# Kernel optimization log

Hardware: AMD Instinct MI355X
Metric: run time of the kernel (lower is better)

Reference implementation:

```python
import jax, jax.numpy as jnp
import numpy as np

N_SAMPLES, N_CHANNELS, LOOKBACK, N_ASSETS = 256, 32, 64, 512
HIDDEN = 32  # hidden_size == n_channels per docstring output shape


def setup_inputs() -> dict:
    key = jax.random.key(0)
    k1, k2, k3, k4, k5 = jax.random.split(key, 5)
    bound = 1.0 / np.sqrt(HIDDEN)  # torch RNNCell init: U(-1/sqrt(H), 1/sqrt(H))
    x = jax.random.normal(k1, (N_SAMPLES, N_CHANNELS, LOOKBACK, N_ASSETS), dtype=jnp.float32)
    W_ih = jax.random.uniform(k2, (HIDDEN, N_CHANNELS), jnp.float32, -bound, bound)
    W_hh = jax.random.uniform(k3, (HIDDEN, HIDDEN), jnp.float32, -bound, bound)
    b_ih = jax.random.uniform(k4, (HIDDEN,), jnp.float32, -bound, bound)
    b_hh = jax.random.uniform(k5, (HIDDEN,), jnp.float32, -bound, bound)
    return {"x": x, "W_ih": W_ih, "W_hh": W_hh, "b_ih": b_ih, "b_hh": b_hh}


def reference(x, W_ih, W_hh, b_ih, b_hh):
    # The original calls self.cell(input) with NO hidden state, so torch.nn.RNNCell
    # uses hx = zeros at EVERY timestep: h_j = tanh(x_j @ W_ih^T + b_ih + 0 @ W_hh^T + b_hh).
    # Hence the W_hh contraction is identically zero and there is no recurrence.
    # hidden_strategy='many2many' -> mean over the lookback axis of the per-step activations.
    # x: (s, c, l, a); W_ih: (h, c) -> pre: (s, h, l, a)
    pre = jnp.einsum('scla,hc->shla', x, W_ih) + (b_ih + b_hh)[None, :, None, None]
    h = jnp.tanh(pre)
    return jnp.mean(h, axis=2)  # (n_samples, hidden_size, n_assets)
```

## Files before the change

kernel.cpp:

```cpp
#include <hip/hip_runtime.h>
#include <hip/hip_bf16.h>

#define NS 256
#define NC 32
#define NL 64
#define NA 512
#define NH 32

typedef float  f32x4  __attribute__((ext_vector_type(4)));
typedef __bf16 bf16x8 __attribute__((ext_vector_type(8)));

__device__ __forceinline__ float fast_tanh(float x) {
    float xc = fminf(fmaxf(x, -9.0f), 9.0f);
    float t = __builtin_amdgcn_exp2f(xc * 2.885390081777927f);
    return (t - 1.0f) * __builtin_amdgcn_rcpf(t + 1.0f);
}

#define GLOAD16(gsrc, ldst) \
  __builtin_amdgcn_global_load_lds((const __attribute__((address_space(1))) void*)(gsrc), \
                                   (__attribute__((address_space(3))) void*)(ldst), 16, 0, 0)

__global__ __launch_bounds__(256, 4) void tcrnn_kernel(
    const float* __restrict__ x,
    const float* __restrict__ Wih,
    const float* __restrict__ bih,
    const float* __restrict__ bhh,
    float* __restrict__ out)
{
    __shared__ float lds[3][2][NC * 64];

    const int tid   = threadIdx.x;
    const int lane  = tid & 63;
    const int w     = tid >> 6;

    const int swz   = ((blockIdx.x & 7) << 8) + (blockIdx.x >> 3);
    const int s     = swz >> 3;
    const int chunk = swz & 7;

    const int n     = lane & 15;
    const int g     = lane >> 4;

    bf16x8 Af[2];
    #pragma unroll
    for (int t = 0; t < 2; ++t) {
        const int h = t * 16 + n;
        const float4 w0 = *reinterpret_cast<const float4*>(Wih + h * NC + g * 8);
        const float4 w1 = *reinterpret_cast<const float4*>(Wih + h * NC + g * 8 + 4);
        Af[t][0] = (__bf16)w0.x; Af[t][1] = (__bf16)w0.y;
        Af[t][2] = (__bf16)w0.z; Af[t][3] = (__bf16)w0.w;
        Af[t][4] = (__bf16)w1.x; Af[t][5] = (__bf16)w1.y;
        Af[t][6] = (__bf16)w1.z; Af[t][7] = (__bf16)w1.w;
    }

    float bias[8];
    #pragma unroll
    for (int t = 0; t < 2; ++t)
        #pragma unroll
        for (int r = 0; r < 4; ++r) {
            const int h = t * 16 + g * 4 + r;
            bias[t * 4 + r] = bih[h] + bhh[h];
        }

    const int st_row = w * 8 + (lane >> 4);
    const int a_st   = chunk * 64 + (((lane & 15) * 4) ^ (w << 4));
    const float* xst = x + (size_t)(s * NC + st_row) * (NL * NA) + a_st;

    const int swz_a = (w * 16 + n) ^ (g << 4);

    f32x4 acc0 = {0.f, 0.f, 0.f, 0.f};
    f32x4 acc1 = {0.f, 0.f, 0.f, 0.f};
    const f32x4 z = {0.f, 0.f, 0.f, 0.f};

    auto stage = [&](int r, int buf) {
        const int l0 = 2 * r;
        #pragma unroll
        for (int p = 0; p < 2; ++p)
            #pragma unroll
            for (int q = 0; q < 2; ++q) {
                const float* gsrc = xst + ((size_t)q * 4 * NL + l0 + p) * NA;
                float* ldst = &lds[buf][p][(w * 8 + q * 4) * 64];
                GLOAD16(gsrc, ldst);
            }
    };

    stage(0, 0);
    stage(1, 1);
    int bc = 0;
    for (int r = 0; r < 32; ++r) {
        if (r > 0) asm volatile("s_barrier" ::: "memory");

        if (r + 2 < 32) {
            const int bs = (bc >= 1) ? bc - 1 : bc + 2;
            stage(r + 2, bs);
            asm volatile("s_waitcnt vmcnt(8)" ::: "memory");
        } else if (r + 1 < 32) {
            asm volatile("s_waitcnt vmcnt(4)" ::: "memory");
        } else {
            asm volatile("s_waitcnt vmcnt(0)" ::: "memory");
        }
        asm volatile("s_barrier" ::: "memory");

        #pragma unroll
        for (int p = 0; p < 2; ++p) {
            const float* base = &lds[bc][p][g * 512 + swz_a];
            bf16x8 B;
            #pragma unroll
            for (int j = 0; j < 8; ++j)
                B[j] = (__bf16)base[j * 64];

            f32x4 pre0 = __builtin_amdgcn_mfma_f32_16x16x32_bf16(Af[0], B, z, 0, 0, 0);
            f32x4 pre1 = __builtin_amdgcn_mfma_f32_16x16x32_bf16(Af[1], B, z, 0, 0, 0);

            #pragma unroll
            for (int r4 = 0; r4 < 4; ++r4) {
                acc0[r4] += fast_tanh(pre0[r4] + bias[r4]);
                acc1[r4] += fast_tanh(pre1[r4] + bias[4 + r4]);
            }
        }
        if (++bc == 3) bc = 0;
    }

    const int a = chunk * 64 + w * 16 + n;
    float* op = out + (size_t)s * (NH * NA) + a;
    #pragma unroll
    for (int r4 = 0; r4 < 4; ++r4) {
        op[(size_t)(g * 4 + r4) * NA]      = acc0[r4] * 0.015625f;
        op[(size_t)(16 + g * 4 + r4) * NA] = acc1[r4] * 0.015625f;
    }
}

extern "C" void kernel_launch(void* const* d_in, const int* in_sizes, int n_in,
                              void* d_out, int out_size, void* d_ws, size_t ws_size,
                              hipStream_t stream) {
    const float* x    = (const float*)d_in[0];
    const float* Wih  = (const float*)d_in[1];
    const float* bih  = (const float*)d_in[3];
    const float* bhh  = (const float*)d_in[4];
    float* out = (float*)d_out;

    dim3 grid(NS * 8);
    dim3 block(256);
    tcrnn_kernel<<<grid, block, 0, stream>>>(x, Wih, bih, bhh, out);
}
```

Baseline: 213.1 us.

## Widen block tile to 256 assets with one-timestep double-buffered staging

Each block now covers 256 assets instead of 64, and the grid shrinks from 2048 to 512 blocks. Each stage loads one timestep per 8 channels as contiguous 1 KB rows into a double buffer, in place of the earlier triple buffer of two timesteps. Each wave holds four accumulator tiles and the launch-bounds occupancy hint drops to 2. The aim is longer contiguous global reads and fewer blocks, at the cost of more registers, fewer waves to hide latency, and a shallower prefetch depth.

```diff
diff --git a/kernel.cpp b/kernel.cpp
--- a/kernel.cpp
+++ b/kernel.cpp
@@ -20,25 +20,23 @@
   __builtin_amdgcn_global_load_lds((const __attribute__((address_space(1))) void*)(gsrc), \
                                    (__attribute__((address_space(3))) void*)(ldst), 16, 0, 0)
 
-__global__ __launch_bounds__(256, 4) void tcrnn_kernel(
+__global__ __launch_bounds__(256, 2) void tcrnn_kernel(
     const float* __restrict__ x,
     const float* __restrict__ Wih,
     const float* __restrict__ bih,
     const float* __restrict__ bhh,
     float* __restrict__ out)
 {
-    __shared__ float lds[3][2][NC * 64];
+    __shared__ float lds[2][NC][256];
 
     const int tid   = threadIdx.x;
     const int lane  = tid & 63;
     const int w     = tid >> 6;
+    const int s     = blockIdx.x >> 1;
+    const int chunk = blockIdx.x & 1;
 
-    const int swz   = ((blockIdx.x & 7) << 8) + (blockIdx.x >> 3);
-    const int s     = swz >> 3;
-    const int chunk = swz & 7;
-
-    const int n     = lane & 15;
-    const int g     = lane >> 4;
+    const int n = lane & 15;
+    const int g = lane >> 4;
 
     bf16x8 Af[2];
     #pragma unroll
@@ -61,71 +59,69 @@
             bias[t * 4 + r] = bih[h] + bhh[h];
         }
 
-    const int st_row = w * 8 + (lane >> 4);
-    const int a_st   = chunk * 64 + (((lane & 15) * 4) ^ (w << 4));
-    const float* xst = x + (size_t)(s * NC + st_row) * (NL * NA) + a_st;
+    const int Xw = (w & 1) << 4;
+    const int lane_off = (lane * 4) ^ Xw;
+    const float* xw = x + (size_t)(s * NC + w * 8) * (NL * NA)
+                        + chunk * 256 + lane_off;
 
-    const int swz_a = (w * 16 + n) ^ (g << 4);
-
-    f32x4 acc0 = {0.f, 0.f, 0.f, 0.f};
-    f32x4 acc1 = {0.f, 0.f, 0.f, 0.f};
-    const f32x4 z = {0.f, 0.f, 0.f, 0.f};
-
-    auto stage = [&](int r, int buf) {
-        const int l0 = 2 * r;
+    auto stage = [&](int l, int buf) {
         #pragma unroll
-        for (int p = 0; p < 2; ++p)
-            #pragma unroll
-            for (int q = 0; q < 2; ++q) {
-                const float* gsrc = xst + ((size_t)q * 4 * NL + l0 + p) * NA;
-                float* ldst = &lds[buf][p][(w * 8 + q * 4) * 64];
-                GLOAD16(gsrc, ldst);
-            }
+        for (int i = 0; i < 8; ++i) {
+            const float* gsrc = xw + ((size_t)i * NL + l) * NA;
+            GLOAD16(gsrc, &lds[buf][w * 8 + i][0]);
+        }
     };
 
+    f32x4 acc[4][2];
+    #pragma unroll
+    for (int t2 = 0; t2 < 4; ++t2) {
+        acc[t2][0] = (f32x4){0.f, 0.f, 0.f, 0.f};
+        acc[t2][1] = (f32x4){0.f, 0.f, 0.f, 0.f};
+    }
+    const f32x4 z = {0.f, 0.f, 0.f, 0.f};
+    const int Xg = (g & 1) << 4;
+
     stage(0, 0);
-    stage(1, 1);
-    int bc = 0;
-    for (int r = 0; r < 32; ++r) {
-        if (r > 0) asm volatile("s_barrier" ::: "memory");
+    for (int l = 0; l < NL; ++l) {
+        if (l > 0) asm volatile("s_barrier" ::: "memory");
 
-        if (r + 2 < 32) {
-            const int bs = (bc >= 1) ? bc - 1 : bc + 2;
-            stage(r + 2, bs);
+        if (l + 1 < NL) {
+            stage(l + 1, (l + 1) & 1);
             asm volatile("s_waitcnt vmcnt(8)" ::: "memory");
-        } else if (r + 1 < 32) {
-            asm volatile("s_waitcnt vmcnt(4)" ::: "memory");
         } else {
             asm volatile("s_waitcnt vmcnt(0)" ::: "memory");
         }
         asm volatile("s_barrier" ::: "memory");
 
         #pragma unroll
-        for (int p = 0; p < 2; ++p) {
-            const float* base = &lds[bc][p][g * 512 + swz_a];
+        for (int t2 = 0; t2 < 4; ++t2) {
+            const int sa = (w * 64 + t2 * 16 + n) ^ Xg;
+            const float* base = &lds[l & 1][g * 8][sa];
             bf16x8 B;
             #pragma unroll
             for (int j = 0; j < 8; ++j)
-                B[j] = (__bf16)base[j * 64];
+                B[j] = (__bf16)base[j * 256];
 
             f32x4 pre0 = __builtin_amdgcn_mfma_f32_16x16x32_bf16(Af[0], B, z, 0, 0, 0);
             f32x4 pre1 = __builtin_amdgcn_mfma_f32_16x16x32_bf16(Af[1], B, z, 0, 0, 0);
 
             #pragma unroll
             for (int r4 = 0; r4 < 4; ++r4) {
-                acc0[r4] += fast_tanh(pre0[r4] + bias[r4]);
-                acc1[r4] += fast_tanh(pre1[r4] + bias[4 + r4]);
+                acc[t2][0][r4] += fast_tanh(pre0[r4] + bias[r4]);
+                acc[t2][1][r4] += fast_tanh(pre1[r4] + bias[4 + r4]);
             }
         }
-        if (++bc == 3) bc = 0;
     }
 
-    const int a = chunk * 64 + w * 16 + n;
-    float* op = out + (size_t)s * (NH * NA) + a;
     #pragma unroll
-    for (int r4 = 0; r4 < 4; ++r4) {
-        op[(size_t)(g * 4 + r4) * NA]      = acc0[r4] * 0.015625f;
-        op[(size_t)(16 + g * 4 + r4) * NA] = acc1[r4] * 0.015625f;
+    for (int t2 = 0; t2 < 4; ++t2) {
+        const int a = chunk * 256 + w * 64 + t2 * 16 + n;
+        float* op = out + (size_t)s * (NH * NA) + a;
+        #pragma unroll
+        for (int r4 = 0; r4 < 4; ++r4) {
+            op[(size_t)(g * 4 + r4) * NA]      = acc[t2][0][r4] * 0.015625f;
+            op[(size_t)(16 + g * 4 + r4) * NA] = acc[t2][1][r4] * 0.015625f;
+        }
     }
 }
 
@@ -138,7 +134,7 @@
     const float* bhh  = (const float*)d_in[4];
     float* out = (float*)d_out;
 
-    dim3 grid(NS * 8);
+    dim3 grid(NS * 2);
     dim3 block(256);
     tcrnn_kernel<<<grid, block, 0, stream>>>(x, Wih, bih, bhh, out);
 }
```

Result: no change. 212.4 us (-0.3%).
